# Optimization experiments

Measured on AMD Instinct MI355X. Metric: run time of the kernel, lower is better.

The kernel has to match this reference:

```python
import jax, jax.numpy as jnp
import numpy as np

B, T, D, H = 64, 1024, 256, 256


def setup_inputs() -> dict:
    key = jax.random.key(0)
    ks = jax.random.split(key, 8)
    s_in = 1.0 / np.sqrt(D)   # ~xavier scale for DxH
    s_h = 1.0 / np.sqrt(H)
    x_seq = jax.random.normal(ks[0], (B, T, D), jnp.float32)
    h_prev = jnp.zeros((B, H), jnp.float32)
    c_prev = jnp.zeros((B, H), jnp.float32)
    W_in = jax.random.normal(ks[1], (D, H), jnp.float32) * s_in
    Wx = jax.random.normal(ks[2], (4, D, H), jnp.float32) * s_in   # gate order f,i,o,g
    Wh = jax.random.normal(ks[3], (4, H, H), jnp.float32) * s_h
    We = jax.random.normal(ks[4], (4, H, H), jnp.float32) * s_h
    b = jnp.zeros((4, H), jnp.float32).at[0].set(1.0)  # forget-gate bias init = 1
    W_out = jax.random.normal(ks[5], (H, D), jnp.float32) * s_h
    b_out = jnp.zeros((D,), jnp.float32)
    return {"x_seq": x_seq, "h_prev": h_prev, "c_prev": c_prev, "W_in": W_in,
            "Wx": Wx, "Wh": Wh, "We": We, "b": b, "W_out": W_out, "b_out": b_out}


def reference(x_seq, h_prev, c_prev, W_in, Wx, Wh, We, b, W_out, b_out):
    # Precompute all input projections once (batched over T):
    xin = jnp.einsum('btd,dh->bth', x_seq, W_in)          # [B,T,H]
    xg = jnp.einsum('btd,kdh->btkh', x_seq, Wx)            # [B,T,4,H]

    def step(carry, inp):
        h, c = carry
        xin_t, xg_t = inp                                  # [B,H], [B,4,H]
        e = xin_t - h                                      # innovation e_t
        pre = (xg_t
               + jnp.einsum('bh,khj->bkj', h, Wh)
               + jnp.einsum('bh,khj->bkj', e, We)
               + b)                                        # [B,4,H]
        f = jax.nn.sigmoid(pre[:, 0])
        i = jax.nn.sigmoid(pre[:, 1])
        o = jax.nn.sigmoid(pre[:, 2])
        g = jnp.tanh(pre[:, 3])
        c_new = f * c + i * g
        h_new = o * jnp.tanh(c_new)
        return (h_new, c_new), (h_new, c_new)

    xin_t = jnp.swapaxes(xin, 0, 1)                        # [T,B,H]
    xg_t = jnp.swapaxes(xg, 0, 1)                          # [T,B,4,H]
    _, (h_seq, c_seq) = jax.lax.scan(step, (h_prev, c_prev), (xin_t, xg_t))
    h_seq = jnp.swapaxes(h_seq, 0, 1)                      # [B,T,H]
    c_seq = jnp.swapaxes(c_seq, 0, 1)
    y_hat = jnp.einsum('bth,hd->btd', h_seq, W_out) + b_out
    return y_hat, h_seq, c_seq
```

## Files before the change

kernel.cpp:

```cpp
#include <hip/hip_runtime.h>
#include <cstdint>
#include <cstddef>


typedef unsigned int   u32;
typedef unsigned short u16;
typedef float  f32x4  __attribute__((ext_vector_type(4)));
typedef short  bf16x8 __attribute__((ext_vector_type(8)));
typedef _Float16 h2_t __attribute__((ext_vector_type(2)));

__device__ __forceinline__ u16 f2bf(float f){
  union { float f; u32 i; } v; v.f = f;
  u32 u = v.i; u32 r = u + 0x7fffu + ((u >> 16) & 1u);
  return (u16)(r >> 16);
}
__device__ __forceinline__ float bf2f(u16 u){
  union { u32 i; float f; } v; v.i = ((u32)u) << 16; return v.f;
}
__device__ __forceinline__ h2_t as_h2(u32 u){
  union { u32 u; h2_t h; } c; c.u = u; return c.h;
}
__device__ __forceinline__ u32 pack_h2(float lo, float hi){
  h2_t h; h.x = (_Float16)lo; h.y = (_Float16)hi;
  union { h2_t h; u32 u; } c; c.h = h; return c.u;
}

#if defined(__has_builtin)
#if __has_builtin(__builtin_amdgcn_fdot2)
#define HAVE_FDOT2 1
#endif
#endif

__device__ __forceinline__ float dot2acc(u32 w, u32 h, float acc){
#ifdef HAVE_FDOT2
  return __builtin_amdgcn_fdot2(as_h2(w), as_h2(h), acc, false);
#else
  h2_t a = as_h2(w), b = as_h2(h);
  acc += (float)a.x * (float)b.x;
  acc += (float)a.y * (float)b.y;
  return acc;
#endif
}

__device__ __forceinline__ float sigf(float x){
  return __builtin_amdgcn_rcpf(1.f + __expf(-x));
}
__device__ __forceinline__ float tanhf_(float x){
  return 2.f * __builtin_amdgcn_rcpf(1.f + __expf(-2.f * x)) - 1.f;
}

__global__ void prep_A(const float* __restrict__ Win, const float* __restrict__ Wx,
                       const float* __restrict__ We, u16* __restrict__ At){
  int n  = blockIdx.x;
  int kg = n >> 8, j = n & 255;
  int k  = threadIdx.x;
  __shared__ float wec[256];
  wec[k] = We[kg * 65536 + k * 256 + j];
  __syncthreads();
  float s = Wx[kg * 65536 + k * 256 + j];
  const float* wrow = Win + k * 256;
  #pragma unroll 8
  for (int m = 0; m < 256; m++) s += wrow[m] * wec[m];
  At[n * 256 + k] = f2bf(s);
}

__global__ void prep_R(const float* __restrict__ Wh, const float* __restrict__ We,
                       u32* __restrict__ Rres, u32* __restrict__ Rstrw){
  int g   = blockIdx.x * 512 + threadIdx.x;
  int k2  = g >> 10, col = g & 1023;
  int kg  = col >> 8, j = col & 255;
  int base = kg * 65536 + (2 * k2) * 256 + j;
  float lo = Wh[base]       - We[base];
  float hi = Wh[base + 256] - We[base + 256];
  u32 u = pack_h2(lo, hi);
  if (col < 512) {
    Rres[k2 * 512 + col] = u;
  } else {
    int q = k2 >> 2, e = k2 & 3;
    Rstrw[(q * 512 + (col - 512)) * 4 + e] = u;
  }
}

__global__ __launch_bounds__(256, 2) void gemm_g(
    const float* __restrict__ X, const u16* __restrict__ At,
    u16* __restrict__ Gc, const float* __restrict__ bg, int t0){
  __shared__ u16 As[64 * 256];
  __shared__ u16 Bs[64 * 256];
  int tid = threadIdx.x;
  int bm = blockIdx.x, bn = blockIdx.y;
  int r = tid >> 2, q = tid & 3;
  int m = bm * 64 + r;
  long srow = (long)(m >> 8) * 1024 + t0 + (m & 255);
  const float* ga = X + srow * 256 + q * 64;
  const u16*   gb = At + ((long)bn * 64 + r) * 256 + q * 64;
  u16* la = As + r * 256 + q * 64;
  u16* lb = Bs + r * 256 + q * 64;
  #pragma unroll
  for (int i = 0; i < 8; i++){
    float4 f0 = *(const float4*)(ga + i * 8);
    float4 f1 = *(const float4*)(ga + i * 8 + 4);
    union { u16 h[8]; uint4 v; } pk;
    pk.h[0] = f2bf(f0.x); pk.h[1] = f2bf(f0.y); pk.h[2] = f2bf(f0.z); pk.h[3] = f2bf(f0.w);
    pk.h[4] = f2bf(f1.x); pk.h[5] = f2bf(f1.y); pk.h[6] = f2bf(f1.z); pk.h[7] = f2bf(f1.w);
    *(uint4*)(la + i * 8) = pk.v;
    *(uint4*)(lb + i * 8) = *(const uint4*)(gb + i * 8);
  }
  __syncthreads();

  int wave = tid >> 6, lane = tid & 63;
  int wm = (wave & 1) * 32, wn = (wave >> 1) * 32;
  int fr = lane & 15, quad = lane >> 4;
  f32x4 acc00 = {0,0,0,0}, acc01 = {0,0,0,0}, acc10 = {0,0,0,0}, acc11 = {0,0,0,0};
  const u16* pa0 = As + (wm + fr) * 256 + quad * 8;
  const u16* pa1 = pa0 + 16 * 256;
  const u16* pb0 = Bs + (wn + fr) * 256 + quad * 8;
  const u16* pb1 = pb0 + 16 * 256;
  #pragma unroll
  for (int k = 0; k < 256; k += 32){
    bf16x8 a0 = *(const bf16x8*)(pa0 + k);
    bf16x8 a1 = *(const bf16x8*)(pa1 + k);
    bf16x8 b0 = *(const bf16x8*)(pb0 + k);
    bf16x8 b1 = *(const bf16x8*)(pb1 + k);
    acc00 = __builtin_amdgcn_mfma_f32_16x16x32_bf16(a0, b0, acc00, 0, 0, 0);
    acc01 = __builtin_amdgcn_mfma_f32_16x16x32_bf16(a0, b1, acc01, 0, 0, 0);
    acc10 = __builtin_amdgcn_mfma_f32_16x16x32_bf16(a1, b0, acc10, 0, 0, 0);
    acc11 = __builtin_amdgcn_mfma_f32_16x16x32_bf16(a1, b1, acc11, 0, 0, 0);
  }
  int cr = quad * 4, cc = fr;
  long rowbase = (long)bm * 64 + wm + cr;
  long colbase = (long)bn * 64 + wn + cc;
  float bias0 = bg[colbase];
  float bias1 = bg[colbase + 16];
  #pragma unroll
  for (int e = 0; e < 4; e++){
    long r0 = rowbase + e, r1 = r0 + 16;
    Gc[r0 * 1024 + colbase]      = f2bf(acc00[e] + bias0);
    Gc[r0 * 1024 + colbase + 16] = f2bf(acc01[e] + bias1);
    Gc[r1 * 1024 + colbase]      = f2bf(acc10[e] + bias0);
    Gc[r1 * 1024 + colbase + 16] = f2bf(acc11[e] + bias1);
  }
}

__global__ __launch_bounds__(256, 2) void gemm_y(
    const float* __restrict__ Hs, const float* __restrict__ Wo,
    float* __restrict__ Y, const float* __restrict__ bo){
  __shared__ u16 As[64 * 256];
  __shared__ u16 Bs[64 * 256];
  int tid = threadIdx.x;
  int bm = blockIdx.x, bn = blockIdx.y;
  int r = tid >> 2, q = tid & 3;
  const float* ga = Hs + ((long)bm * 64 + r) * 256 + q * 64;
  u16* la = As + r * 256 + q * 64;
  #pragma unroll
  for (int i = 0; i < 8; i++){
    float4 f0 = *(const float4*)(ga + i * 8);
    float4 f1 = *(const float4*)(ga + i * 8 + 4);
    union { u16 h[8]; uint4 v; } pk;
    pk.h[0] = f2bf(f0.x); pk.h[1] = f2bf(f0.y); pk.h[2] = f2bf(f0.z); pk.h[3] = f2bf(f0.w);
    pk.h[4] = f2bf(f1.x); pk.h[5] = f2bf(f1.y); pk.h[6] = f2bf(f1.z); pk.h[7] = f2bf(f1.w);
    *(uint4*)(la + i * 8) = pk.v;
  }
  int ncol = bn * 64 + r;
  u16* lb = Bs + r * 256 + q * 64;
  #pragma unroll 8
  for (int i = 0; i < 64; i++) lb[i] = f2bf(Wo[(q * 64 + i) * 256 + ncol]);
  __syncthreads();

  int wave = tid >> 6, lane = tid & 63;
  int wm = (wave & 1) * 32, wn = (wave >> 1) * 32;
  int fr = lane & 15, quad = lane >> 4;
  f32x4 acc00 = {0,0,0,0}, acc01 = {0,0,0,0}, acc10 = {0,0,0,0}, acc11 = {0,0,0,0};
  const u16* pa0 = As + (wm + fr) * 256 + quad * 8;
  const u16* pa1 = pa0 + 16 * 256;
  const u16* pb0 = Bs + (wn + fr) * 256 + quad * 8;
  const u16* pb1 = pb0 + 16 * 256;
  #pragma unroll
  for (int k = 0; k < 256; k += 32){
    bf16x8 a0 = *(const bf16x8*)(pa0 + k);
    bf16x8 a1 = *(const bf16x8*)(pa1 + k);
    bf16x8 b0 = *(const bf16x8*)(pb0 + k);
    bf16x8 b1 = *(const bf16x8*)(pb1 + k);
    acc00 = __builtin_amdgcn_mfma_f32_16x16x32_bf16(a0, b0, acc00, 0, 0, 0);
    acc01 = __builtin_amdgcn_mfma_f32_16x16x32_bf16(a0, b1, acc01, 0, 0, 0);
    acc10 = __builtin_amdgcn_mfma_f32_16x16x32_bf16(a1, b0, acc10, 0, 0, 0);
    acc11 = __builtin_amdgcn_mfma_f32_16x16x32_bf16(a1, b1, acc11, 0, 0, 0);
  }
  int cr = quad * 4, cc = fr;
  long rowbase = (long)bm * 64 + wm + cr;
  long colbase = (long)bn * 64 + wn + cc;
  float bias0 = bo[colbase];
  float bias1 = bo[colbase + 16];
  #pragma unroll
  for (int e = 0; e < 4; e++){
    long r0 = rowbase + e, r1 = r0 + 16;
    Y[r0 * 256 + colbase]      = acc00[e] + bias0;
    Y[r0 * 256 + colbase + 16] = acc01[e] + bias1;
    Y[r1 * 256 + colbase]      = acc10[e] + bias0;
    Y[r1 * 256 + colbase + 16] = acc11[e] + bias1;
  }
}

__global__ __launch_bounds__(512, 2) void scan_chunk(
    const u32* __restrict__ Rres, const uint4* __restrict__ Rstr,
    const u16* __restrict__ Gc,
    const float* __restrict__ h0, const float* __restrict__ c0,
    u32* __restrict__ stateH, float* __restrict__ stateC,
    float* __restrict__ hseq, float* __restrict__ cseq, int t0){
  const int CT = 256;
  int b = blockIdx.x;
  int j = threadIdx.x;

  u32 w[128];
  #pragma unroll
  for (int k2 = 0; k2 < 128; k2++) w[k2] = Rres[k2 * 512 + j];

  __shared__ __align__(16) u32 hbuf[128];
  __shared__ float xch[1024];

  float cst = 0.f;
  if (t0 == 0){
    if (j < 128) hbuf[j] = pack_h2(h0[b * 256 + 2 * j], h0[b * 256 + 2 * j + 1]);
    if (j < 256) cst = c0[b * 256 + j];
  } else {
    if (j < 128) hbuf[j] = stateH[b * 128 + j];
    if (j < 256) cst = stateC[b * 256 + j];
  }

  const u16* Grow = Gc + (size_t)b * CT * 1024;
  u16 ga = Grow[j], gb = Grow[512 + j];
  const uint4* Rsj = Rstr + j;
  __syncthreads();

  for (int tt = 0; tt < CT; tt++){
    const u16* Gn = Grow + (size_t)(tt + 1 < CT ? tt + 1 : tt) * 1024;
    u16 gan = Gn[j], gbn = Gn[512 + j];

    float acc0 = bf2f(ga), acc1 = bf2f(gb);
    #pragma unroll
    for (int qk = 0; qk < 32; qk++){
      uint4 ws4 = Rsj[qk * 512];
      uint4 hh  = *(const uint4*)(hbuf + qk * 4);
      acc0 = dot2acc(w[4*qk + 0], hh.x, acc0);
      acc0 = dot2acc(w[4*qk + 1], hh.y, acc0);
      acc0 = dot2acc(w[4*qk + 2], hh.z, acc0);
      acc0 = dot2acc(w[4*qk + 3], hh.w, acc0);
      acc1 = dot2acc(ws4.x, hh.x, acc1);
      acc1 = dot2acc(ws4.y, hh.y, acc1);
      acc1 = dot2acc(ws4.z, hh.z, acc1);
      acc1 = dot2acc(ws4.w, hh.w, acc1);
    }
    xch[j] = acc0; xch[512 + j] = acc1;
    __syncthreads();

    if (j < 256){
      float f  = sigf(xch[j]);
      float ii = sigf(xch[256 + j]);
      float o  = sigf(xch[512 + j]);
      float g  = tanhf_(xch[768 + j]);
      cst = f * cst + ii * g;
      float hv = o * tanhf_(cst);
      size_t orow = ((size_t)b * 1024 + t0 + tt) * 256 + j;
      hseq[orow] = hv;
      cseq[orow] = cst;
      xch[j] = hv;
    }
    __syncthreads();

    if (j < 128) hbuf[j] = pack_h2(xch[2 * j], xch[2 * j + 1]);
    ga = gan; gb = gbn;
    __syncthreads();
  }

  if (j < 128) stateH[b * 128 + j] = hbuf[j];
  if (j < 256) stateC[b * 256 + j] = cst;
}

extern "C" void kernel_launch(void* const* d_in, const int* in_sizes, int n_in,
                              void* d_out, int out_size, void* d_ws, size_t ws_size,
                              hipStream_t stream){
  const float* x   = (const float*)d_in[0];
  const float* h0  = (const float*)d_in[1];
  const float* c0  = (const float*)d_in[2];
  const float* Win = (const float*)d_in[3];
  const float* Wx  = (const float*)d_in[4];
  const float* Wh  = (const float*)d_in[5];
  const float* We  = (const float*)d_in[6];
  const float* bg  = (const float*)d_in[7];
  const float* Wo  = (const float*)d_in[8];
  const float* bo  = (const float*)d_in[9];

  float* y    = (float*)d_out;
  float* hseq = y + 16777216;
  float* cseq = y + 33554432;

  char* yb = (char*)d_out;
  u16*   Gc     = (u16*)(yb);
  u16*   At     = (u16*)(yb + 33554432);
  u32*   Rres   = (u32*)(yb + 34078720);
  uint4* Rstr   = (uint4*)(yb + 34340864);
  u32*   stateH = (u32*)(yb + 34603008);
  float* stateC = (float*)(yb + 34635776);

  prep_A<<<1024, 256, 0, stream>>>(Win, Wx, We, At);
  prep_R<<<256, 512, 0, stream>>>(Wh, We, Rres, (u32*)Rstr);

  for (int c = 0; c < 4; c++){
    int t0 = c * 256;
    gemm_g<<<dim3(256, 16), 256, 0, stream>>>(x, At, Gc, bg, t0);
    scan_chunk<<<64, 512, 0, stream>>>(Rres, Rstr, Gc, h0, c0,
                                       stateH, stateC, hseq, cseq, t0);
  }

  gemm_y<<<dim3(1024, 4), 256, 0, stream>>>(hseq, Wo, y, bo);
}
```

Baseline: 3.909 ms.

## Keep scan recurrent weights in registers and LDS; pair gates per thread, double-buffer h

```diff
diff --git a/kernel.cpp b/kernel.cpp
--- a/kernel.cpp
+++ b/kernel.cpp
@@ -65,7 +65,7 @@
 }
 
 __global__ void prep_R(const float* __restrict__ Wh, const float* __restrict__ We,
-                       u32* __restrict__ Rres, u32* __restrict__ Rstrw){
+                       u32* __restrict__ Rres, u32* __restrict__ Rstr2){
   int g   = blockIdx.x * 512 + threadIdx.x;
   int k2  = g >> 10, col = g & 1023;
   int kg  = col >> 8, j = col & 255;
@@ -73,12 +73,8 @@
   float lo = Wh[base]       - We[base];
   float hi = Wh[base + 256] - We[base + 256];
   u32 u = pack_h2(lo, hi);
-  if (col < 512) {
-    Rres[k2 * 512 + col] = u;
-  } else {
-    int q = k2 >> 2, e = k2 & 3;
-    Rstrw[(q * 512 + (col - 512)) * 4 + e] = u;
-  }
+  if (col < 512) Rres[k2 * 512 + col] = u;
+  else           Rstr2[k2 * 512 + (col - 512)] = u;
 }
 
 __global__ __launch_bounds__(256, 2) void gemm_g(
@@ -201,77 +197,102 @@
 }
 
 __global__ __launch_bounds__(512, 2) void scan_chunk(
-    const u32* __restrict__ Rres, const uint4* __restrict__ Rstr,
+    const u32* __restrict__ Rres, const u32* __restrict__ Rstr2,
     const u16* __restrict__ Gc,
     const float* __restrict__ h0, const float* __restrict__ c0,
     u32* __restrict__ stateH, float* __restrict__ stateC,
     float* __restrict__ hseq, float* __restrict__ cseq, int t0){
   const int CT = 256;
+  const int LSTR = 68;
   int b = blockIdx.x;
   int j = threadIdx.x;
 
+  __shared__ __align__(16) u32 Lw[512 * LSTR];
+  __shared__ __align__(16) u16 hb[2][256];
+  __shared__ float xch[256];
+
+  u32* mys = Lw + j * LSTR;
+
   u32 w[128];
   #pragma unroll
   for (int k2 = 0; k2 < 128; k2++) w[k2] = Rres[k2 * 512 + j];
-
-  __shared__ __align__(16) u32 hbuf[128];
-  __shared__ float xch[1024];
+  u32 w2[64];
+  #pragma unroll
+  for (int i = 0; i < 64; i++) w2[i] = Rstr2[i * 512 + j];
+  #pragma unroll
+  for (int i = 0; i < 64; i++) mys[i] = Rstr2[(64 + i) * 512 + j];
 
   float cst = 0.f;
   if (t0 == 0){
-    if (j < 128) hbuf[j] = pack_h2(h0[b * 256 + 2 * j], h0[b * 256 + 2 * j + 1]);
+    if (j < 128) ((u32*)hb[0])[j] = pack_h2(h0[b * 256 + 2 * j], h0[b * 256 + 2 * j + 1]);
     if (j < 256) cst = c0[b * 256 + j];
   } else {
-    if (j < 128) hbuf[j] = stateH[b * 128 + j];
+    if (j < 128) ((u32*)hb[0])[j] = stateH[b * 128 + j];
     if (j < 256) cst = stateC[b * 256 + j];
   }
 
   const u16* Grow = Gc + (size_t)b * CT * 1024;
   u16 ga = Grow[j], gb = Grow[512 + j];
-  const uint4* Rsj = Rstr + j;
   __syncthreads();
 
+  int p = 0;
   for (int tt = 0; tt < CT; tt++){
     const u16* Gn = Grow + (size_t)(tt + 1 < CT ? tt + 1 : tt) * 1024;
     u16 gan = Gn[j], gbn = Gn[512 + j];
 
     float acc0 = bf2f(ga), acc1 = bf2f(gb);
+    const u16* hrow = hb[p];
     #pragma unroll
-    for (int qk = 0; qk < 32; qk++){
-      uint4 ws4 = Rsj[qk * 512];
-      uint4 hh  = *(const uint4*)(hbuf + qk * 4);
-      acc0 = dot2acc(w[4*qk + 0], hh.x, acc0);
-      acc0 = dot2acc(w[4*qk + 1], hh.y, acc0);
-      acc0 = dot2acc(w[4*qk + 2], hh.z, acc0);
-      acc0 = dot2acc(w[4*qk + 3], hh.w, acc0);
-      acc1 = dot2acc(ws4.x, hh.x, acc1);
-      acc1 = dot2acc(ws4.y, hh.y, acc1);
-      acc1 = dot2acc(ws4.z, hh.z, acc1);
-      acc1 = dot2acc(ws4.w, hh.w, acc1);
+    for (int qk = 0; qk < 16; qk++){
+      uint4 hh = *(const uint4*)(hrow + qk * 8);
+      acc0 = dot2acc(w[4 * qk + 0], hh.x, acc0);
+      acc0 = dot2acc(w[4 * qk + 1], hh.y, acc0);
+      acc0 = dot2acc(w[4 * qk + 2], hh.z, acc0);
+      acc0 = dot2acc(w[4 * qk + 3], hh.w, acc0);
+      acc1 = dot2acc(w2[4 * qk + 0], hh.x, acc1);
+      acc1 = dot2acc(w2[4 * qk + 1], hh.y, acc1);
+      acc1 = dot2acc(w2[4 * qk + 2], hh.z, acc1);
+      acc1 = dot2acc(w2[4 * qk + 3], hh.w, acc1);
     }
-    xch[j] = acc0; xch[512 + j] = acc1;
+    #pragma unroll
+    for (int qk = 0; qk < 16; qk++){
+      uint4 hh = *(const uint4*)(hrow + 128 + qk * 8);
+      uint4 ws = *(const uint4*)(mys + 4 * qk);
+      acc0 = dot2acc(w[64 + 4 * qk + 0], hh.x, acc0);
+      acc0 = dot2acc(w[64 + 4 * qk + 1], hh.y, acc0);
+      acc0 = dot2acc(w[64 + 4 * qk + 2], hh.z, acc0);
+      acc0 = dot2acc(w[64 + 4 * qk + 3], hh.w, acc0);
+      acc1 = dot2acc(ws.x, hh.x, acc1);
+      acc1 = dot2acc(ws.y, hh.y, acc1);
+      acc1 = dot2acc(ws.z, hh.z, acc1);
+      acc1 = dot2acc(ws.w, hh.w, acc1);
+    }
+
+    float f = 0.f, o = 0.f;
+    if (j >= 256){
+      xch[j - 256] = sigf(acc0) * tanhf_(acc1);
+    } else {
+      f = sigf(acc0);
+      o = sigf(acc1);
+    }
     __syncthreads();
 
     if (j < 256){
-      float f  = sigf(xch[j]);
-      float ii = sigf(xch[256 + j]);
-      float o  = sigf(xch[512 + j]);
-      float g  = tanhf_(xch[768 + j]);
-      cst = f * cst + ii * g;
+      cst = f * cst + xch[j];
       float hv = o * tanhf_(cst);
       size_t orow = ((size_t)b * 1024 + t0 + tt) * 256 + j;
       hseq[orow] = hv;
       cseq[orow] = cst;
-      xch[j] = hv;
+      union { _Float16 h; u16 u; } cv; cv.h = (_Float16)hv;
+      hb[p ^ 1][j] = cv.u;
     }
     __syncthreads();
 
-    if (j < 128) hbuf[j] = pack_h2(xch[2 * j], xch[2 * j + 1]);
     ga = gan; gb = gbn;
-    __syncthreads();
-  }
-
-  if (j < 128) stateH[b * 128 + j] = hbuf[j];
+    p ^= 1;
+  }
+
+  if (j < 128) stateH[b * 128 + j] = ((u32*)hb[p])[j];
   if (j < 256) stateC[b * 256 + j] = cst;
 }
 
@@ -297,17 +318,17 @@
   u16*   Gc     = (u16*)(yb);
   u16*   At     = (u16*)(yb + 33554432);
   u32*   Rres   = (u32*)(yb + 34078720);
-  uint4* Rstr   = (uint4*)(yb + 34340864);
+  u32*   Rstr2  = (u32*)(yb + 34340864);
   u32*   stateH = (u32*)(yb + 34603008);
   float* stateC = (float*)(yb + 34635776);
 
   prep_A<<<1024, 256, 0, stream>>>(Win, Wx, We, At);
-  prep_R<<<256, 512, 0, stream>>>(Wh, We, Rres, (u32*)Rstr);
+  prep_R<<<256, 512, 0, stream>>>(Wh, We, Rres, Rstr2);
 
   for (int c = 0; c < 4; c++){
     int t0 = c * 256;
     gemm_g<<<dim3(256, 16), 256, 0, stream>>>(x, At, Gc, bg, t0);
-    scan_chunk<<<64, 512, 0, stream>>>(Rres, Rstr, Gc, h0, c0,
+    scan_chunk<<<64, 512, 0, stream>>>(Rres, Rstr2, Gc, h0, c0,
                                        stateH, stateC, hseq, cseq, t0);
   }
 
```

Result: slower. 9.584 ms (+145.2%).

## Restructure LSTM scan: one thread per gate column, readlane hidden-state broadcast

Applied to the files above, without the earlier changes.

```diff
diff --git a/kernel.cpp b/kernel.cpp
--- a/kernel.cpp
+++ b/kernel.cpp
@@ -29,6 +29,12 @@
 #if __has_builtin(__builtin_amdgcn_fdot2)
 #define HAVE_FDOT2 1
 #endif
+#if __has_builtin(__builtin_amdgcn_readlane)
+#define RDL(v, l) ((u32)__builtin_amdgcn_readlane((int)(v), (l)))
+#endif
+#endif
+#ifndef RDL
+#define RDL(v, l) ((u32)__shfl((int)(v), (l), 64))
 #endif
 
 __device__ __forceinline__ float dot2acc(u32 w, u32 h, float acc){
@@ -65,7 +71,8 @@
 }
 
 __global__ void prep_R(const float* __restrict__ Wh, const float* __restrict__ We,
-                       u32* __restrict__ Rres, u32* __restrict__ Rstrw){
+                       u32* __restrict__ Rreg, u32* __restrict__ R1,
+                       u32* __restrict__ R2){
   int g   = blockIdx.x * 512 + threadIdx.x;
   int k2  = g >> 10, col = g & 1023;
   int kg  = col >> 8, j = col & 255;
@@ -73,11 +80,11 @@
   float lo = Wh[base]       - We[base];
   float hi = Wh[base + 256] - We[base + 256];
   u32 u = pack_h2(lo, hi);
-  if (col < 512) {
-    Rres[k2 * 512 + col] = u;
-  } else {
-    int q = k2 >> 2, e = k2 & 3;
-    Rstrw[(q * 512 + (col - 512)) * 4 + e] = u;
+  if (k2 < 64)      Rreg[k2 * 1024 + col] = u;
+  else if (k2 < 96) R1[(k2 - 64) * 1024 + col] = u;
+  else {
+    int q = (k2 - 96) >> 2, e = (k2 - 96) & 3;
+    R2[(q * 1024 + col) * 4 + e] = u;
   }
 }
 
@@ -200,79 +207,153 @@
   }
 }
 
-__global__ __launch_bounds__(512, 2) void scan_chunk(
-    const u32* __restrict__ Rres, const uint4* __restrict__ Rstr,
-    const u16* __restrict__ Gc,
+__global__ __launch_bounds__(1024, 4) void scan_chunk(
+    const u32* __restrict__ Rreg, const u32* __restrict__ R1,
+    const uint4* __restrict__ R2v, const u16* __restrict__ Gc,
     const float* __restrict__ h0, const float* __restrict__ c0,
-    u32* __restrict__ stateH, float* __restrict__ stateC,
     float* __restrict__ hseq, float* __restrict__ cseq, int t0){
   const int CT = 256;
   int b = blockIdx.x;
   int j = threadIdx.x;
-
-  u32 w[128];
-  #pragma unroll
-  for (int k2 = 0; k2 < 128; k2++) w[k2] = Rres[k2 * 512 + j];
-
-  __shared__ __align__(16) u32 hbuf[128];
-  __shared__ float xch[1024];
-
-  float cst = 0.f;
+  int l = j & 63;
+  int wv = j >> 6;
+  int sw = (j & 7);
+
+  __shared__ __align__(16) u32 Lw[1024 * 32];
+  __shared__ float xg2[2][1024];
+
+  u32* mys = Lw + j * 32;
+
+  u32 w[64];
+  #pragma unroll
+  for (int kp = 0; kp < 64; kp++) w[kp] = Rreg[kp * 1024 + j];
+  #pragma unroll
+  for (int e = 0; e < 8; e++){
+    uint4 t;
+    t.x = R1[(4 * e + 0) * 1024 + j];
+    t.y = R1[(4 * e + 1) * 1024 + j];
+    t.z = R1[(4 * e + 2) * 1024 + j];
+    t.w = R1[(4 * e + 3) * 1024 + j];
+    *(uint4*)(mys + ((e ^ sw) << 2)) = t;
+  }
+
+  u32 hA, hB;
+  float cA0, cA1, cB0, cB1;
   if (t0 == 0){
-    if (j < 128) hbuf[j] = pack_h2(h0[b * 256 + 2 * j], h0[b * 256 + 2 * j + 1]);
-    if (j < 256) cst = c0[b * 256 + j];
+    const float* hp = h0 + b * 256;
+    const float* cp = c0 + b * 256;
+    hA = pack_h2(hp[2 * l], hp[2 * l + 1]);
+    hB = pack_h2(hp[128 + 2 * l], hp[129 + 2 * l]);
+    cA0 = cp[2 * l]; cA1 = cp[2 * l + 1];
+    cB0 = cp[128 + 2 * l]; cB1 = cp[129 + 2 * l];
   } else {
-    if (j < 128) hbuf[j] = stateH[b * 128 + j];
-    if (j < 256) cst = stateC[b * 256 + j];
+    size_t prow = ((size_t)b * 1024 + t0 - 1) * 256;
+    hA = pack_h2(hseq[prow + 2 * l], hseq[prow + 2 * l + 1]);
+    hB = pack_h2(hseq[prow + 128 + 2 * l], hseq[prow + 129 + 2 * l]);
+    cA0 = cseq[prow + 2 * l]; cA1 = cseq[prow + 2 * l + 1];
+    cB0 = cseq[prow + 128 + 2 * l]; cB1 = cseq[prow + 129 + 2 * l];
   }
 
   const u16* Grow = Gc + (size_t)b * CT * 1024;
-  u16 ga = Grow[j], gb = Grow[512 + j];
-  const uint4* Rsj = Rstr + j;
+  u16 ga = Grow[j];
   __syncthreads();
 
+  int pp = 0;
   for (int tt = 0; tt < CT; tt++){
+    uint4 s0 = R2v[0 * 1024 + j];
+    uint4 s1 = R2v[1 * 1024 + j];
+    uint4 s2 = R2v[2 * 1024 + j];
+    uint4 s3 = R2v[3 * 1024 + j];
     const u16* Gn = Grow + (size_t)(tt + 1 < CT ? tt + 1 : tt) * 1024;
-    u16 gan = Gn[j], gbn = Gn[512 + j];
-
-    float acc0 = bf2f(ga), acc1 = bf2f(gb);
+    u16 gan = Gn[j];
+
+    float a0 = bf2f(ga), a1 = 0.f;
+
     #pragma unroll
-    for (int qk = 0; qk < 32; qk++){
-      uint4 ws4 = Rsj[qk * 512];
-      uint4 hh  = *(const uint4*)(hbuf + qk * 4);
-      acc0 = dot2acc(w[4*qk + 0], hh.x, acc0);
-      acc0 = dot2acc(w[4*qk + 1], hh.y, acc0);
-      acc0 = dot2acc(w[4*qk + 2], hh.z, acc0);
-      acc0 = dot2acc(w[4*qk + 3], hh.w, acc0);
-      acc1 = dot2acc(ws4.x, hh.x, acc1);
-      acc1 = dot2acc(ws4.y, hh.y, acc1);
-      acc1 = dot2acc(ws4.z, hh.z, acc1);
-      acc1 = dot2acc(ws4.w, hh.w, acc1);
+    for (int kp = 0; kp < 64; kp += 2){
+      a0 = dot2acc(w[kp],     RDL(hA, kp),     a0);
+      a1 = dot2acc(w[kp + 1], RDL(hA, kp + 1), a1);
     }
-    xch[j] = acc0; xch[512 + j] = acc1;
+    #pragma unroll
+    for (int e = 0; e < 8; e++){
+      uint4 ws = *(const uint4*)(mys + ((e ^ sw) << 2));
+      a0 = dot2acc(ws.x, RDL(hB, 4 * e + 0), a0);
+      a1 = dot2acc(ws.y, RDL(hB, 4 * e + 1), a1);
+      a0 = dot2acc(ws.z, RDL(hB, 4 * e + 2), a0);
+      a1 = dot2acc(ws.w, RDL(hB, 4 * e + 3), a1);
+    }
+    uint4 s4 = R2v[4 * 1024 + j];
+    uint4 s5 = R2v[5 * 1024 + j];
+    uint4 s6 = R2v[6 * 1024 + j];
+    uint4 s7 = R2v[7 * 1024 + j];
+    a0 = dot2acc(s0.x, RDL(hB, 32), a0);
+    a1 = dot2acc(s0.y, RDL(hB, 33), a1);
+    a0 = dot2acc(s0.z, RDL(hB, 34), a0);
+    a1 = dot2acc(s0.w, RDL(hB, 35), a1);
+    a0 = dot2acc(s1.x, RDL(hB, 36), a0);
+    a1 = dot2acc(s1.y, RDL(hB, 37), a1);
+    a0 = dot2acc(s1.z, RDL(hB, 38), a0);
+    a1 = dot2acc(s1.w, RDL(hB, 39), a1);
+    a0 = dot2acc(s2.x, RDL(hB, 40), a0);
+    a1 = dot2acc(s2.y, RDL(hB, 41), a1);
+    a0 = dot2acc(s2.z, RDL(hB, 42), a0);
+    a1 = dot2acc(s2.w, RDL(hB, 43), a1);
+    a0 = dot2acc(s3.x, RDL(hB, 44), a0);
+    a1 = dot2acc(s3.y, RDL(hB, 45), a1);
+    a0 = dot2acc(s3.z, RDL(hB, 46), a0);
+    a1 = dot2acc(s3.w, RDL(hB, 47), a1);
+    a0 = dot2acc(s4.x, RDL(hB, 48), a0);
+    a1 = dot2acc(s4.y, RDL(hB, 49), a1);
+    a0 = dot2acc(s4.z, RDL(hB, 50), a0);
+    a1 = dot2acc(s4.w, RDL(hB, 51), a1);
+    a0 = dot2acc(s5.x, RDL(hB, 52), a0);
+    a1 = dot2acc(s5.y, RDL(hB, 53), a1);
+    a0 = dot2acc(s5.z, RDL(hB, 54), a0);
+    a1 = dot2acc(s5.w, RDL(hB, 55), a1);
+    a0 = dot2acc(s6.x, RDL(hB, 56), a0);
+    a1 = dot2acc(s6.y, RDL(hB, 57), a1);
+    a0 = dot2acc(s6.z, RDL(hB, 58), a0);
+    a1 = dot2acc(s6.w, RDL(hB, 59), a1);
+    a0 = dot2acc(s7.x, RDL(hB, 60), a0);
+    a1 = dot2acc(s7.y, RDL(hB, 61), a1);
+    a0 = dot2acc(s7.z, RDL(hB, 62), a0);
+    a1 = dot2acc(s7.w, RDL(hB, 63), a1);
+
+    float acc = a0 + a1;
+    float gv = (j < 768) ? sigf(acc) : tanhf_(acc);
+    xg2[pp][j] = gv;
     __syncthreads();
 
-    if (j < 256){
-      float f  = sigf(xch[j]);
-      float ii = sigf(xch[256 + j]);
-      float o  = sigf(xch[512 + j]);
-      float g  = tanhf_(xch[768 + j]);
-      cst = f * cst + ii * g;
-      float hv = o * tanhf_(cst);
-      size_t orow = ((size_t)b * 1024 + t0 + tt) * 256 + j;
-      hseq[orow] = hv;
-      cseq[orow] = cst;
-      xch[j] = hv;
+    const float* xb = xg2[pp];
+    float2 f1_ = *(const float2*)(xb +   0 + 2 * l);
+    float2 i1_ = *(const float2*)(xb + 256 + 2 * l);
+    float2 o1_ = *(const float2*)(xb + 512 + 2 * l);
+    float2 g1_ = *(const float2*)(xb + 768 + 2 * l);
+    float2 f2_ = *(const float2*)(xb + 128 + 2 * l);
+    float2 i2_ = *(const float2*)(xb + 384 + 2 * l);
+    float2 o2_ = *(const float2*)(xb + 640 + 2 * l);
+    float2 g2_ = *(const float2*)(xb + 896 + 2 * l);
+
+    cA0 = f1_.x * cA0 + i1_.x * g1_.x;  float h0v = o1_.x * tanhf_(cA0);
+    cA1 = f1_.y * cA1 + i1_.y * g1_.y;  float h1v = o1_.y * tanhf_(cA1);
+    cB0 = f2_.x * cB0 + i2_.x * g2_.x;  float h2v = o2_.x * tanhf_(cB0);
+    cB1 = f2_.y * cB1 + i2_.y * g2_.y;  float h3v = o2_.y * tanhf_(cB1);
+    hA = pack_h2(h0v, h1v);
+    hB = pack_h2(h2v, h3v);
+
+    if (wv == 0){
+      size_t orow = ((size_t)b * 1024 + t0 + tt) * 256;
+      float2 vh0 = {h0v, h1v}, vh1 = {h2v, h3v};
+      float2 vc0 = {cA0, cA1}, vc1 = {cB0, cB1};
+      *(float2*)(hseq + orow + 2 * l)       = vh0;
+      *(float2*)(hseq + orow + 128 + 2 * l) = vh1;
+      *(float2*)(cseq + orow + 2 * l)       = vc0;
+      *(float2*)(cseq + orow + 128 + 2 * l) = vc1;
     }
-    __syncthreads();
-
-    if (j < 128) hbuf[j] = pack_h2(xch[2 * j], xch[2 * j + 1]);
-    ga = gan; gb = gbn;
-    __syncthreads();
-  }
-
-  if (j < 128) stateH[b * 128 + j] = hbuf[j];
-  if (j < 256) stateC[b * 256 + j] = cst;
+
+    ga = gan;
+    pp ^= 1;
+  }
 }
 
 extern "C" void kernel_launch(void* const* d_in, const int* in_sizes, int n_in,
@@ -296,19 +377,18 @@
   char* yb = (char*)d_out;
   u16*   Gc     = (u16*)(yb);
   u16*   At     = (u16*)(yb + 33554432);
-  u32*   Rres   = (u32*)(yb + 34078720);
-  uint4* Rstr   = (uint4*)(yb + 34340864);
-  u32*   stateH = (u32*)(yb + 34603008);
-  float* stateC = (float*)(yb + 34635776);
+  u32*   Rreg   = (u32*)(yb + 34078720);
+  u32*   R1     = (u32*)(yb + 34340864);
+  u32*   R2     = (u32*)(yb + 34471936);
 
   prep_A<<<1024, 256, 0, stream>>>(Win, Wx, We, At);
-  prep_R<<<256, 512, 0, stream>>>(Wh, We, Rres, (u32*)Rstr);
+  prep_R<<<256, 512, 0, stream>>>(Wh, We, Rreg, R1, R2);
 
   for (int c = 0; c < 4; c++){
     int t0 = c * 256;
     gemm_g<<<dim3(256, 16), 256, 0, stream>>>(x, At, Gc, bg, t0);
-    scan_chunk<<<64, 512, 0, stream>>>(Rres, Rstr, Gc, h0, c0,
-                                       stateH, stateC, hseq, cseq, t0);
+    scan_chunk<<<64, 1024, 0, stream>>>(Rreg, R1, (const uint4*)R2, Gc, h0, c0,
+                                        hseq, cseq, t0);
   }
 
   gemm_y<<<dim3(1024, 4), 256, 0, stream>>>(hseq, Wo, y, bo);
```

Measured after the change: 3.447 ms. 1.13x faster.
